# Optimization experiments

Hardware: AMD Instinct MI355X
Metric: run time of the kernel (lower is better)

## Reference

```python
import jax, jax.numpy as jnp
import numpy as np

BETA = 0.9      # membrane decay
THRESH = 1.0    # firing threshold


def _lif(x):
    """Leaky integrate-and-fire over leading time axis. x: (T, ..., C) -> spikes (T, ..., C)."""
    def step(mem, xt):
        mem = BETA * mem + xt
        s = (mem > THRESH).astype(xt.dtype)
        mem = mem - s * THRESH  # soft reset
        return mem, s
    _, spikes = jax.lax.scan(step, jnp.zeros_like(x[0]), x)
    return spikes


def setup_inputs() -> dict:
    key = jax.random.key(0)
    k1, k2, k3, k4, k5 = jax.random.split(key, 5)
    T, N, D = 4, 8192, 1024
    E, EF, TOPK = 8, 512, 2  # expert_ff = d_ff // n_experts = 4096 // 8
    x = jax.random.normal(k1, (T, N, D), dtype=jnp.float32)
    expert_indices = jax.random.randint(k2, (N, TOPK), 0, E)
    expert_weights = jax.random.uniform(k3, (N, TOPK), dtype=jnp.float32)
    up_w = jax.random.normal(k4, (E, EF, D), dtype=jnp.float32) * 0.02   # Linear(d_model, ef).weight
    down_w = jax.random.normal(k5, (E, D, EF), dtype=jnp.float32) * 0.02  # Linear(ef, d_model).weight
    return {"x": x, "expert_indices": expert_indices, "expert_weights": expert_weights,
            "up_w": up_w, "down_w": down_w}


def reference(x, expert_indices, expert_weights, up_w, down_w):
    T, N, D = x.shape
    E = up_w.shape[0]
    # Dense combine weights W[n, e] = sum_k weights[n, k] * (indices[n, k] == e)
    W = jnp.zeros((N, E), dtype=x.dtype).at[
        jnp.arange(N)[:, None], expert_indices].add(expert_weights)
    out = jnp.zeros_like(x)
    for e in range(E):  # fixed small loop over experts
        h = _lif(jnp.einsum('tnd,fd->tnf', x, up_w[e]))   # up-proj + LIF hidden
        o = _lif(jnp.einsum('tnf,df->tnd', h, down_w[e]))  # down-proj + LIF output
        out = out + o * W[:, e][None, :, None]             # weighted combine (0 for inactive)
    return out
```

## Files before the change

kernel.cpp:

```cpp
#include <hip/hip_runtime.h>
#include <stdint.h>

#define T_STEPS 4
#define NTOK    8192
#define DMODEL  1024
#define NEXP    8
#define EFF     512
#define BMT     128
#define CAPTOT  (2*NTOK + NEXP*BMT)

typedef __attribute__((ext_vector_type(8))) short bf8_t;
typedef __attribute__((ext_vector_type(4))) float f32x4;

#define MFMA(a,b,c) __builtin_amdgcn_mfma_f32_16x16x32_bf16((a),(b),(c),0,0,0)

#define SWZC(r, c) ((((c) ^ (((r) >> 1) & 3))) * 8)

typedef __attribute__((address_space(3))) unsigned int lds_uint;
typedef const __attribute__((address_space(1))) unsigned int glb_uint;
__device__ __forceinline__ void dma16(const void* g, void* l) {
    __builtin_amdgcn_global_load_lds((glb_uint*)g, (lds_uint*)l, 16, 0, 0);
}
#define S_BARRIER() __builtin_amdgcn_s_barrier()
#define SFENCE()    __builtin_amdgcn_sched_barrier(0)


__device__ __forceinline__ unsigned short bf16rn(float f) {
    unsigned u = __float_as_uint(f);
    unsigned r = u + 0x7fffu + ((u >> 16) & 1u);
    return (unsigned short)(r >> 16);
}
__device__ __forceinline__ float bf2f(unsigned short h) {
    return __uint_as_float(((unsigned)h) << 16);
}
__device__ __forceinline__ unsigned pk(unsigned short a, unsigned short b) {
    return (unsigned)a | ((unsigned)b << 16);
}

__device__ __forceinline__ void split8v(float4 va, float4 vb,
                                        unsigned short* d0, unsigned short* d1,
                                        unsigned short* d2) {
    float v[8];
    *(float4*)&v[0] = va;
    *(float4*)&v[4] = vb;
    unsigned short h[8], m[8], l[8];
#pragma unroll
    for (int i = 0; i < 8; ++i) {
        unsigned short a = bf16rn(v[i]);
        float r1 = v[i] - bf2f(a);
        unsigned short b = bf16rn(r1);
        float r2 = r1 - bf2f(b);
        h[i] = a; m[i] = b; l[i] = bf16rn(r2);
    }
    *(uint4*)d0 = make_uint4(pk(h[0],h[1]), pk(h[2],h[3]), pk(h[4],h[5]), pk(h[6],h[7]));
    *(uint4*)d1 = make_uint4(pk(m[0],m[1]), pk(m[2],m[3]), pk(m[4],m[5]), pk(m[6],m[7]));
    *(uint4*)d2 = make_uint4(pk(l[0],l[1]), pk(l[2],l[3]), pk(l[4],l[5]), pk(l[6],l[7]));
}

__device__ __forceinline__ void stage8_3limb(const float* __restrict__ src,
                                             unsigned short* d0, unsigned short* d1,
                                             unsigned short* d2) {
    float4 va = *(const float4*)(src + 0);
    float4 vb = *(const float4*)(src + 4);
    split8v(va, vb, d0, d1, d2);
}


__global__ void k_split(const float* __restrict__ w, unsigned short* __restrict__ h,
                        unsigned short* __restrict__ m, unsigned short* __restrict__ l) {
    size_t i = (size_t)(blockIdx.x * blockDim.x + threadIdx.x) * 8;
    stage8_3limb(w + i, h + i, m + i, l + i);
}


__global__ void k_count(const int* __restrict__ idx, int* __restrict__ counts) {
    int n = blockIdx.x * blockDim.x + threadIdx.x;
    if (n >= NTOK) return;
    int e0 = idx[2*n], e1 = idx[2*n+1];
    atomicAdd(&counts[e0], 1);
    if (e1 != e0) atomicAdd(&counts[e1], 1);
}

__global__ void k_prefix(const int* __restrict__ counts, int* __restrict__ offsets) {
    if (threadIdx.x == 0) {
        int o = 0;
        for (int e = 0; e < NEXP; ++e) {
            offsets[e] = o;
            o += (counts[e] + BMT - 1) / BMT * BMT;
        }
        offsets[NEXP] = o;
    }
}

__global__ void k_fill(const int* __restrict__ idx, const float* __restrict__ wts,
                       const int* __restrict__ offsets, int* __restrict__ cursors,
                       int* __restrict__ tok, float* __restrict__ wgt) {
    int n = blockIdx.x * blockDim.x + threadIdx.x;
    if (n >= NTOK) return;
    int e0 = idx[2*n], e1 = idx[2*n+1];
    float w0 = wts[2*n], w1 = wts[2*n+1];
    if (e0 == e1) w0 = __fadd_rn(w0, w1);
    int p0 = offsets[e0] + atomicAdd(&cursors[e0], 1);
    tok[p0] = n; wgt[p0] = w0;
    if (e1 != e0) {
        int p1 = offsets[e1] + atomicAdd(&cursors[e1], 1);
        tok[p1] = n; wgt[p1] = w1;
    }
}


__global__ __launch_bounds__(256, 2)
void k_up(const float* __restrict__ x,
          const unsigned short* __restrict__ uwh, const unsigned short* __restrict__ uwm,
          const unsigned short* __restrict__ uwl,
          const int* __restrict__ offsets, const int* __restrict__ tok,
          unsigned short* __restrict__ spk) {
    const int m0 = blockIdx.x * BMT;
    const int ft = blockIdx.y;
    if (m0 >= offsets[NEXP]) return;
    int e = 0;
    for (int i = 1; i < NEXP; ++i) if (m0 >= offsets[i]) e = i;

    __shared__ __align__(16) unsigned short As[3][128][32];
    __shared__ __align__(16) unsigned short Bs[2][3][128][32];

    const int tid  = threadIdx.x;
    const int lane = tid & 63, wid = tid >> 6;
    const int quad = lane >> 4, l16 = lane & 15;
    const int mw = (wid & 1) * 64, nw = (wid >> 1) * 64;

    const int r = tid >> 1, half = tid & 1;
    const int c0 = SWZC(r, half*2 + 0);
    const int c1 = SWZC(r, half*2 + 1);
    const int tokA = tok[m0 + r];
    const float* xbase = x + (size_t)tokA * DMODEL + half * 16;

    const unsigned short* wlimb[3] = { uwh, uwm, uwl };
    const size_t wrow0 = ((size_t)e * EFF + ft * 128) * DMODEL;
    const int drow  = lane >> 2;
    const int dclog = (lane & 3) ^ ((lane >> 3) & 3);

    const int kq = SWZC(l16, quad);

    f32x4 mem[4][4];
#pragma unroll
    for (int i = 0; i < 4; ++i)
#pragma unroll
        for (int j = 0; j < 4; ++j) mem[i][j] = (f32x4){0.f,0.f,0.f,0.f};

#pragma unroll
    for (int j = 0; j < 6; ++j) {
        const int limb = j >> 1, rh = j & 1;
        dma16(wlimb[limb] + wrow0 + (size_t)(rh*64 + wid*16 + drow) * DMODEL + dclog*8,
              &Bs[0][limb][rh*64 + wid*16][0]);
    }
    float4 pa[4];
#pragma unroll
    for (int i = 0; i < 4; ++i) pa[i] = ((const float4*)xbase)[i];

    int cur = 0;
    for (int t = 0; t < T_STEPS; ++t) {
        f32x4 acc[4][4];
#pragma unroll
        for (int i = 0; i < 4; ++i)
#pragma unroll
            for (int j = 0; j < 4; ++j) acc[i][j] = (f32x4){0.f,0.f,0.f,0.f};

        const float* xrow = xbase + (size_t)t * NTOK * DMODEL;

        for (int kc = 0; kc < DMODEL; kc += 32) {
            const bool last = (t == T_STEPS - 1) && (kc == DMODEL - 32);
            asm volatile("s_waitcnt lgkmcnt(0)" ::: "memory");
            SFENCE();
            S_BARRIER();
            SFENCE();
            if (!last) {
                const int nkk = (kc == DMODEL - 32) ? 0 : kc + 32;
#pragma unroll
                for (int j = 0; j < 6; ++j) {
                    const int limb = j >> 1, rh = j & 1;
                    dma16(wlimb[limb] + wrow0 + (size_t)(rh*64 + wid*16 + drow) * DMODEL
                              + nkk + dclog*8,
                          &Bs[cur ^ 1][limb][rh*64 + wid*16][0]);
                }
            }
            split8v(pa[0], pa[1], &As[0][r][c0], &As[1][r][c0], &As[2][r][c0]);
            split8v(pa[2], pa[3], &As[0][r][c1], &As[1][r][c1], &As[2][r][c1]);
            if (!last) {
                const float* nxtA = (kc == DMODEL - 32)
                    ? xbase + (size_t)(t + 1) * NTOK * DMODEL
                    : xrow + kc + 32;
#pragma unroll
                for (int i = 0; i < 4; ++i) pa[i] = ((const float4*)nxtA)[i];
                asm volatile("s_waitcnt vmcnt(10) lgkmcnt(0)" ::: "memory");
            } else {
                asm volatile("s_waitcnt vmcnt(0) lgkmcnt(0)" ::: "memory");
            }
            SFENCE();
            S_BARRIER();
            SFENCE();

            bf8_t bh[4], bm[4], bl[4];
#pragma unroll
            for (int nt = 0; nt < 4; ++nt) {
                const int nr = nw + nt*16 + l16;
                bh[nt] = *(const bf8_t*)&Bs[cur][0][nr][kq];
                bm[nt] = *(const bf8_t*)&Bs[cur][1][nr][kq];
                bl[nt] = *(const bf8_t*)&Bs[cur][2][nr][kq];
            }
#pragma unroll
            for (int mt = 0; mt < 4; ++mt) {
                const int mr = mw + mt*16 + l16;
                bf8_t ah = *(const bf8_t*)&As[0][mr][kq];
                bf8_t am = *(const bf8_t*)&As[1][mr][kq];
                bf8_t al = *(const bf8_t*)&As[2][mr][kq];
#pragma unroll
                for (int nt = 0; nt < 4; ++nt) {
                    f32x4 c = acc[mt][nt];
                    c = MFMA(ah, bh[nt], c);
                    c = MFMA(am, bh[nt], c);
                    c = MFMA(ah, bm[nt], c);
                    c = MFMA(am, bm[nt], c);
                    c = MFMA(al, bh[nt], c);
                    c = MFMA(ah, bl[nt], c);
                    acc[mt][nt] = c;
                }
            }
            cur ^= 1;
        }

#pragma unroll
        for (int mt = 0; mt < 4; ++mt)
#pragma unroll
            for (int nt = 0; nt < 4; ++nt)
#pragma unroll
                for (int reg = 0; reg < 4; ++reg) {
                    float mv = __fadd_rn(__fmul_rn(0.9f, mem[mt][nt][reg]), acc[mt][nt][reg]);
                    bool s = mv > 1.0f;
                    mem[mt][nt][reg] = __fsub_rn(mv, s ? 1.0f : 0.0f);
                    int row = m0 + mw + mt*16 + quad*4 + reg;
                    int col = ft*128 + nw + nt*16 + l16;
                    spk[((size_t)t * CAPTOT + row) * EFF + col] = s ? 0x3F80u : 0u;
                }
    }
}


__global__ __launch_bounds__(256, 2)
void k_dn(const unsigned short* __restrict__ spk,
          const unsigned short* __restrict__ dwh, const unsigned short* __restrict__ dwm,
          const unsigned short* __restrict__ dwl,
          const int* __restrict__ offsets, const int* __restrict__ tok,
          const float* __restrict__ wgt, float* __restrict__ out) {
    const int m0 = blockIdx.x * BMT;
    const int dt = blockIdx.y;
    if (m0 >= offsets[NEXP]) return;
    int e = 0;
    for (int i = 1; i < NEXP; ++i) if (m0 >= offsets[i]) e = i;

    __shared__ __align__(16) unsigned short As[2][128][32];
    __shared__ __align__(16) unsigned short Bs[2][3][128][32];

    const int tid  = threadIdx.x;
    const int lane = tid & 63, wid = tid >> 6;
    const int quad = lane >> 4, l16 = lane & 15;
    const int mw = (wid & 1) * 64, nw = (wid >> 1) * 64;

    const unsigned short* dlimb[3] = { dwh, dwm, dwl };
    const size_t drow0 = ((size_t)e * DMODEL + dt * 128) * EFF;
    const int drow  = lane >> 2;
    const int dclog = (lane & 3) ^ ((lane >> 3) & 3);

    const int kq = SWZC(l16, quad);

    f32x4 mem[4][4];
#pragma unroll
    for (int i = 0; i < 4; ++i)
#pragma unroll
        for (int j = 0; j < 4; ++j) mem[i][j] = (f32x4){0.f,0.f,0.f,0.f};

#pragma unroll
    for (int j2 = 0; j2 < 2; ++j2) {
        const int row = j2*64 + wid*16 + drow;
        dma16(spk + ((size_t)0 * CAPTOT + m0 + row) * EFF + dclog*8,
              &As[0][j2*64 + wid*16][0]);
    }
#pragma unroll
    for (int j = 0; j < 6; ++j) {
        const int limb = j >> 1, rh = j & 1;
        dma16(dlimb[limb] + drow0 + (size_t)(rh*64 + wid*16 + drow) * EFF + dclog*8,
              &Bs[0][limb][rh*64 + wid*16][0]);
    }

    int cur = 0;
    for (int t = 0; t < T_STEPS; ++t) {
        f32x4 acc[4][4];
#pragma unroll
        for (int i = 0; i < 4; ++i)
#pragma unroll
            for (int j = 0; j < 4; ++j) acc[i][j] = (f32x4){0.f,0.f,0.f,0.f};

        for (int kc = 0; kc < EFF; kc += 32) {
            const bool last = (t == T_STEPS - 1) && (kc == EFF - 32);
            asm volatile("s_waitcnt lgkmcnt(0)" ::: "memory");
            SFENCE();
            S_BARRIER();
            SFENCE();
            if (!last) {
                int ntt = t, nkk = kc + 32;
                if (nkk == EFF) { nkk = 0; ntt = t + 1; }
#pragma unroll
                for (int j2 = 0; j2 < 2; ++j2) {
                    const int row = j2*64 + wid*16 + drow;
                    dma16(spk + ((size_t)ntt * CAPTOT + m0 + row) * EFF + nkk + dclog*8,
                          &As[cur ^ 1][j2*64 + wid*16][0]);
                }
#pragma unroll
                for (int j = 0; j < 6; ++j) {
                    const int limb = j >> 1, rh = j & 1;
                    dma16(dlimb[limb] + drow0 + (size_t)(rh*64 + wid*16 + drow) * EFF
                              + nkk + dclog*8,
                          &Bs[cur ^ 1][limb][rh*64 + wid*16][0]);
                }
                asm volatile("s_waitcnt vmcnt(8)" ::: "memory");
            } else {
                asm volatile("s_waitcnt vmcnt(0)" ::: "memory");
            }
            SFENCE();
            S_BARRIER();
            SFENCE();

            bf8_t bh[4], bm[4], bl[4];
#pragma unroll
            for (int nt = 0; nt < 4; ++nt) {
                const int nr = nw + nt*16 + l16;
                bh[nt] = *(const bf8_t*)&Bs[cur][0][nr][kq];
                bm[nt] = *(const bf8_t*)&Bs[cur][1][nr][kq];
                bl[nt] = *(const bf8_t*)&Bs[cur][2][nr][kq];
            }
#pragma unroll
            for (int mt = 0; mt < 4; ++mt) {
                const int mr = mw + mt*16 + l16;
                bf8_t a = *(const bf8_t*)&As[cur][mr][kq];
#pragma unroll
                for (int nt = 0; nt < 4; ++nt) {
                    f32x4 c = acc[mt][nt];
                    c = MFMA(a, bh[nt], c);
                    c = MFMA(a, bm[nt], c);
                    c = MFMA(a, bl[nt], c);
                    acc[mt][nt] = c;
                }
            }
            cur ^= 1;
        }

#pragma unroll
        for (int mt = 0; mt < 4; ++mt) {
            const int rbase = m0 + mw + mt*16 + quad*4;
#pragma unroll
            for (int reg = 0; reg < 4; ++reg) {
                const int   n = tok[rbase + reg];
                const float w = wgt[rbase + reg];
#pragma unroll
                for (int nt = 0; nt < 4; ++nt) {
                    float mv = __fadd_rn(__fmul_rn(0.9f, mem[mt][nt][reg]), acc[mt][nt][reg]);
                    bool s = mv > 1.0f;
                    mem[mt][nt][reg] = __fsub_rn(mv, s ? 1.0f : 0.0f);
                    if (s && w != 0.0f) {
                        int col = dt*128 + nw + nt*16 + l16;
                        atomicAdd(out + ((size_t)t * NTOK + n) * DMODEL + col, w);
                    }
                }
            }
        }
    }
}


extern "C" void kernel_launch(void* const* d_in, const int* in_sizes, int n_in,
                              void* d_out, int out_size, void* d_ws, size_t ws_size,
                              hipStream_t stream) {
    const float* x      = (const float*)d_in[0];
    const int*   idx    = (const int*)  d_in[1];
    const float* wts    = (const float*)d_in[2];
    const float* up_w   = (const float*)d_in[3];
    const float* down_w = (const float*)d_in[4];
    float* out = (float*)d_out;

    char* ws = (char*)d_ws;
    int*   counts  = (int*)(ws + 0);
    int*   cursors = (int*)(ws + 32);
    int*   offsets = (int*)(ws + 64);
    int*   tok     = (int*)(ws + 128);
    float* wgt     = (float*)(ws + 128 + (size_t)CAPTOT * 4);
    unsigned short* spk = (unsigned short*)(ws + 128 + (size_t)CAPTOT * 8);

    const size_t WSPK = (size_t)T_STEPS * CAPTOT * EFF * 2;
    size_t base2 = 128 + (size_t)CAPTOT * 8 + WSPK;
    base2 = (base2 + 511) & ~(size_t)511;
    const size_t WLIMB = (size_t)NEXP * EFF * DMODEL * 2;
    unsigned short* uwh = (unsigned short*)(ws + base2);
    unsigned short* uwm = (unsigned short*)(ws + base2 + 1*WLIMB);
    unsigned short* uwl = (unsigned short*)(ws + base2 + 2*WLIMB);
    unsigned short* dwh = (unsigned short*)(ws + base2 + 3*WLIMB);
    unsigned short* dwm = (unsigned short*)(ws + base2 + 4*WLIMB);
    unsigned short* dwl = (unsigned short*)(ws + base2 + 5*WLIMB);

    hipMemsetAsync(ws, 0, 128 + (size_t)CAPTOT * 8, stream);
    hipMemsetAsync(out, 0, (size_t)out_size * sizeof(float), stream);

    const int nsplit = NEXP * EFF * DMODEL / 8 / 256;
    k_split<<<nsplit, 256, 0, stream>>>(up_w,   uwh, uwm, uwl);
    k_split<<<nsplit, 256, 0, stream>>>(down_w, dwh, dwm, dwl);

    k_count <<<(NTOK + 255) / 256, 256, 0, stream>>>(idx, counts);
    k_prefix<<<1, 64, 0, stream>>>(counts, offsets);
    k_fill  <<<(NTOK + 255) / 256, 256, 0, stream>>>(idx, wts, offsets, cursors, tok, wgt);

    dim3 gup(CAPTOT / BMT, EFF / 128);
    k_up<<<gup, 256, 0, stream>>>(x, uwh, uwm, uwl, offsets, tok, spk);

    dim3 gdn(CAPTOT / BMT, DMODEL / 128);
    k_dn<<<gdn, 256, 0, stream>>>(spk, dwh, dwm, dwl, offsets, tok, wgt, out);
}
```

Baseline: 960.1 us.

## Pre-split activations into bf16 limbs and DMA them directly into LDS

Adds a pre-pass that splits all of x into three bf16 limb arrays in the workspace, and the up-projection now loads A tiles with global-to-LDS DMA instead of per-thread float loads and in-kernel splitting. This takes the VALU split work and register staging off the GEMM's critical path. The cost is an extra full pass over x and extra workspace traffic. It also remaps block indices with a swizzle so that consecutive blocks spread across M tiles. The A DMA is issued in the same iteration it is consumed, so there is less prefetch overlap than before.

```diff
diff --git a/kernel.cpp b/kernel.cpp
--- a/kernel.cpp
+++ b/kernel.cpp
@@ -24,6 +24,8 @@
 #define S_BARRIER() __builtin_amdgcn_s_barrier()
 #define SFENCE()    __builtin_amdgcn_sched_barrier(0)
 
+__device__ __forceinline__ int swz_mb(int bx) { return (bx & 7) * 17 + (bx >> 3); }
+
 
 __device__ __forceinline__ unsigned short bf16rn(float f) {
     unsigned u = __float_as_uint(f);
@@ -37,12 +39,12 @@
     return (unsigned)a | ((unsigned)b << 16);
 }
 
-__device__ __forceinline__ void split8v(float4 va, float4 vb,
-                                        unsigned short* d0, unsigned short* d1,
-                                        unsigned short* d2) {
+__device__ __forceinline__ void stage8_3limb(const float* __restrict__ src,
+                                             unsigned short* d0, unsigned short* d1,
+                                             unsigned short* d2) {
     float v[8];
-    *(float4*)&v[0] = va;
-    *(float4*)&v[4] = vb;
+    *(float4*)&v[0] = *(const float4*)(src + 0);
+    *(float4*)&v[4] = *(const float4*)(src + 4);
     unsigned short h[8], m[8], l[8];
 #pragma unroll
     for (int i = 0; i < 8; ++i) {
@@ -55,14 +57,6 @@
     *(uint4*)d0 = make_uint4(pk(h[0],h[1]), pk(h[2],h[3]), pk(h[4],h[5]), pk(h[6],h[7]));
     *(uint4*)d1 = make_uint4(pk(m[0],m[1]), pk(m[2],m[3]), pk(m[4],m[5]), pk(m[6],m[7]));
     *(uint4*)d2 = make_uint4(pk(l[0],l[1]), pk(l[2],l[3]), pk(l[4],l[5]), pk(l[6],l[7]));
-}
-
-__device__ __forceinline__ void stage8_3limb(const float* __restrict__ src,
-                                             unsigned short* d0, unsigned short* d1,
-                                             unsigned short* d2) {
-    float4 va = *(const float4*)(src + 0);
-    float4 vb = *(const float4*)(src + 4);
-    split8v(va, vb, d0, d1, d2);
 }
 
 
@@ -110,12 +104,13 @@
 
 
 __global__ __launch_bounds__(256, 2)
-void k_up(const float* __restrict__ x,
+void k_up(const unsigned short* __restrict__ xh, const unsigned short* __restrict__ xm,
+          const unsigned short* __restrict__ xl,
           const unsigned short* __restrict__ uwh, const unsigned short* __restrict__ uwm,
           const unsigned short* __restrict__ uwl,
           const int* __restrict__ offsets, const int* __restrict__ tok,
           unsigned short* __restrict__ spk) {
-    const int m0 = blockIdx.x * BMT;
+    const int m0 = swz_mb(blockIdx.x) * BMT;
     const int ft = blockIdx.y;
     if (m0 >= offsets[NEXP]) return;
     int e = 0;
@@ -129,16 +124,13 @@
     const int quad = lane >> 4, l16 = lane & 15;
     const int mw = (wid & 1) * 64, nw = (wid >> 1) * 64;
 
-    const int r = tid >> 1, half = tid & 1;
-    const int c0 = SWZC(r, half*2 + 0);
-    const int c1 = SWZC(r, half*2 + 1);
-    const int tokA = tok[m0 + r];
-    const float* xbase = x + (size_t)tokA * DMODEL + half * 16;
-
-    const unsigned short* wlimb[3] = { uwh, uwm, uwl };
-    const size_t wrow0 = ((size_t)e * EFF + ft * 128) * DMODEL;
     const int drow  = lane >> 2;
     const int dclog = (lane & 3) ^ ((lane >> 3) & 3);
+    const unsigned short* wlimb[3] = { uwh, uwm, uwl };
+    const unsigned short* xlimb[3] = { xh, xm, xl };
+    const size_t wrow0 = ((size_t)e * EFF + ft * 128) * DMODEL;
+    const int tok0 = tok[m0 + wid*16 + drow];
+    const int tok1 = tok[m0 + 64 + wid*16 + drow];
 
     const int kq = SWZC(l16, quad);
 
@@ -154,9 +146,6 @@
         dma16(wlimb[limb] + wrow0 + (size_t)(rh*64 + wid*16 + drow) * DMODEL + dclog*8,
               &Bs[0][limb][rh*64 + wid*16][0]);
     }
-    float4 pa[4];
-#pragma unroll
-    for (int i = 0; i < 4; ++i) pa[i] = ((const float4*)xbase)[i];
 
     int cur = 0;
     for (int t = 0; t < T_STEPS; ++t) {
@@ -166,14 +155,19 @@
 #pragma unroll
             for (int j = 0; j < 4; ++j) acc[i][j] = (f32x4){0.f,0.f,0.f,0.f};
 
-        const float* xrow = xbase + (size_t)t * NTOK * DMODEL;
-
         for (int kc = 0; kc < DMODEL; kc += 32) {
             const bool last = (t == T_STEPS - 1) && (kc == DMODEL - 32);
             asm volatile("s_waitcnt lgkmcnt(0)" ::: "memory");
             SFENCE();
             S_BARRIER();
             SFENCE();
+#pragma unroll
+            for (int j = 0; j < 6; ++j) {
+                const int limb = j >> 1, rh = j & 1;
+                const int tk = rh ? tok1 : tok0;
+                dma16(xlimb[limb] + ((size_t)t * NTOK + tk) * DMODEL + kc + dclog*8,
+                      &As[limb][rh*64 + wid*16][0]);
+            }
             if (!last) {
                 const int nkk = (kc == DMODEL - 32) ? 0 : kc + 32;
 #pragma unroll
@@ -183,18 +177,9 @@
                               + nkk + dclog*8,
                           &Bs[cur ^ 1][limb][rh*64 + wid*16][0]);
                 }
-            }
-            split8v(pa[0], pa[1], &As[0][r][c0], &As[1][r][c0], &As[2][r][c0]);
-            split8v(pa[2], pa[3], &As[0][r][c1], &As[1][r][c1], &As[2][r][c1]);
-            if (!last) {
-                const float* nxtA = (kc == DMODEL - 32)
-                    ? xbase + (size_t)(t + 1) * NTOK * DMODEL
-                    : xrow + kc + 32;
-#pragma unroll
-                for (int i = 0; i < 4; ++i) pa[i] = ((const float4*)nxtA)[i];
-                asm volatile("s_waitcnt vmcnt(10) lgkmcnt(0)" ::: "memory");
+                asm volatile("s_waitcnt vmcnt(6)" ::: "memory");
             } else {
-                asm volatile("s_waitcnt vmcnt(0) lgkmcnt(0)" ::: "memory");
+                asm volatile("s_waitcnt vmcnt(0)" ::: "memory");
             }
             SFENCE();
             S_BARRIER();
@@ -252,7 +237,7 @@
           const unsigned short* __restrict__ dwl,
           const int* __restrict__ offsets, const int* __restrict__ tok,
           const float* __restrict__ wgt, float* __restrict__ out) {
-    const int m0 = blockIdx.x * BMT;
+    const int m0 = swz_mb(blockIdx.x) * BMT;
     const int dt = blockIdx.y;
     if (m0 >= offsets[NEXP]) return;
     int e = 0;
@@ -405,6 +390,11 @@
     unsigned short* dwh = (unsigned short*)(ws + base2 + 3*WLIMB);
     unsigned short* dwm = (unsigned short*)(ws + base2 + 4*WLIMB);
     unsigned short* dwl = (unsigned short*)(ws + base2 + 5*WLIMB);
+    size_t base3 = base2 + 6*WLIMB;
+    const size_t XLIMB = (size_t)T_STEPS * NTOK * DMODEL * 2;
+    unsigned short* xh = (unsigned short*)(ws + base3);
+    unsigned short* xm = (unsigned short*)(ws + base3 + 1*XLIMB);
+    unsigned short* xl = (unsigned short*)(ws + base3 + 2*XLIMB);
 
     hipMemsetAsync(ws, 0, 128 + (size_t)CAPTOT * 8, stream);
     hipMemsetAsync(out, 0, (size_t)out_size * sizeof(float), stream);
@@ -412,13 +402,15 @@
     const int nsplit = NEXP * EFF * DMODEL / 8 / 256;
     k_split<<<nsplit, 256, 0, stream>>>(up_w,   uwh, uwm, uwl);
     k_split<<<nsplit, 256, 0, stream>>>(down_w, dwh, dwm, dwl);
+    const int nsplitx = T_STEPS * NTOK * DMODEL / 8 / 256;
+    k_split<<<nsplitx, 256, 0, stream>>>(x, xh, xm, xl);
 
     k_count <<<(NTOK + 255) / 256, 256, 0, stream>>>(idx, counts);
     k_prefix<<<1, 64, 0, stream>>>(counts, offsets);
     k_fill  <<<(NTOK + 255) / 256, 256, 0, stream>>>(idx, wts, offsets, cursors, tok, wgt);
 
     dim3 gup(CAPTOT / BMT, EFF / 128);
-    k_up<<<gup, 256, 0, stream>>>(x, uwh, uwm, uwl, offsets, tok, spk);
+    k_up<<<gup, 256, 0, stream>>>(xh, xm, xl, uwh, uwm, uwl, offsets, tok, spk);
 
     dim3 gdn(CAPTOT / BMT, DMODEL / 128);
     k_dn<<<gdn, 256, 0, stream>>>(spk, dwh, dwm, dwl, offsets, tok, wgt, out);
```

New measurement: 1.235 ms. +28.7%, slower.

## Widen down-proj K tile to 64, single-buffer weights, swizzle blocks, raise MFMA priority

Applied to the files above, without the earlier changes.

In the down-projection kernel the K step grows from 32 to 64 with a new 8-way LDS swizzle. The weight limbs are now single-buffered and loaded inside the current iteration after the first barrier, instead of being prefetched one step ahead. Only the spike tile stays double-buffered. Both kernels remap block indices so neighbouring blocks are spread across experts, and raise wave priority during the MFMA section. The goal is fewer barriers per K and better scheduling, but weight-load latency is no longer hidden behind compute.

```diff
diff --git a/kernel.cpp b/kernel.cpp
--- a/kernel.cpp
+++ b/kernel.cpp
@@ -14,7 +14,8 @@
 
 #define MFMA(a,b,c) __builtin_amdgcn_mfma_f32_16x16x32_bf16((a),(b),(c),0,0,0)
 
-#define SWZC(r, c) ((((c) ^ (((r) >> 1) & 3))) * 8)
+#define SWZC(r, c)  ((((c) ^ (((r) >> 1) & 3))) * 8)
+#define SWZ64(r, c) ((((c) ^ ((r) & 7))) * 8)
 
 typedef __attribute__((address_space(3))) unsigned int lds_uint;
 typedef const __attribute__((address_space(1))) unsigned int glb_uint;
@@ -23,6 +24,8 @@
 }
 #define S_BARRIER() __builtin_amdgcn_s_barrier()
 #define SFENCE()    __builtin_amdgcn_sched_barrier(0)
+
+__device__ __forceinline__ int swz_mb(int bx) { return (bx & 7) * 17 + (bx >> 3); }
 
 
 __device__ __forceinline__ unsigned short bf16rn(float f) {
@@ -115,7 +118,7 @@
           const unsigned short* __restrict__ uwl,
           const int* __restrict__ offsets, const int* __restrict__ tok,
           unsigned short* __restrict__ spk) {
-    const int m0 = blockIdx.x * BMT;
+    const int m0 = swz_mb(blockIdx.x) * BMT;
     const int ft = blockIdx.y;
     if (m0 >= offsets[NEXP]) return;
     int e = 0;
@@ -208,6 +211,7 @@
                 bm[nt] = *(const bf8_t*)&Bs[cur][1][nr][kq];
                 bl[nt] = *(const bf8_t*)&Bs[cur][2][nr][kq];
             }
+            __builtin_amdgcn_s_setprio(1);
 #pragma unroll
             for (int mt = 0; mt < 4; ++mt) {
                 const int mr = mw + mt*16 + l16;
@@ -226,6 +230,7 @@
                     acc[mt][nt] = c;
                 }
             }
+            __builtin_amdgcn_s_setprio(0);
             cur ^= 1;
         }
 
@@ -252,14 +257,14 @@
           const unsigned short* __restrict__ dwl,
           const int* __restrict__ offsets, const int* __restrict__ tok,
           const float* __restrict__ wgt, float* __restrict__ out) {
-    const int m0 = blockIdx.x * BMT;
+    const int m0 = swz_mb(blockIdx.x) * BMT;
     const int dt = blockIdx.y;
     if (m0 >= offsets[NEXP]) return;
     int e = 0;
     for (int i = 1; i < NEXP; ++i) if (m0 >= offsets[i]) e = i;
 
-    __shared__ __align__(16) unsigned short As[2][128][32];
-    __shared__ __align__(16) unsigned short Bs[2][3][128][32];
+    __shared__ __align__(16) unsigned short As[2][128][64];
+    __shared__ __align__(16) unsigned short Bs[3][128][64];
 
     const int tid  = threadIdx.x;
     const int lane = tid & 63, wid = tid >> 6;
@@ -268,10 +273,8 @@
 
     const unsigned short* dlimb[3] = { dwh, dwm, dwl };
     const size_t drow0 = ((size_t)e * DMODEL + dt * 128) * EFF;
-    const int drow  = lane >> 2;
-    const int dclog = (lane & 3) ^ ((lane >> 3) & 3);
-
-    const int kq = SWZC(l16, quad);
+    const int drow8 = lane >> 3;
+    const int dclog = (lane & 7) ^ ((lane >> 3) & 7);
 
     f32x4 mem[4][4];
 #pragma unroll
@@ -280,16 +283,10 @@
         for (int j = 0; j < 4; ++j) mem[i][j] = (f32x4){0.f,0.f,0.f,0.f};
 
 #pragma unroll
-    for (int j2 = 0; j2 < 2; ++j2) {
-        const int row = j2*64 + wid*16 + drow;
-        dma16(spk + ((size_t)0 * CAPTOT + m0 + row) * EFF + dclog*8,
-              &As[0][j2*64 + wid*16][0]);
-    }
-#pragma unroll
-    for (int j = 0; j < 6; ++j) {
-        const int limb = j >> 1, rh = j & 1;
-        dma16(dlimb[limb] + drow0 + (size_t)(rh*64 + wid*16 + drow) * EFF + dclog*8,
-              &Bs[0][limb][rh*64 + wid*16][0]);
+    for (int j2 = 0; j2 < 4; ++j2) {
+        const int rowb = wid*32 + j2*8;
+        dma16(spk + ((size_t)(m0 + rowb + drow8)) * EFF + dclog*8,
+              &As[0][rowb][0]);
     }
 
     int cur = 0;
@@ -300,29 +297,30 @@
 #pragma unroll
             for (int j = 0; j < 4; ++j) acc[i][j] = (f32x4){0.f,0.f,0.f,0.f};
 
-        for (int kc = 0; kc < EFF; kc += 32) {
-            const bool last = (t == T_STEPS - 1) && (kc == EFF - 32);
+        for (int kc = 0; kc < EFF; kc += 64) {
+            const bool last = (t == T_STEPS - 1) && (kc == EFF - 64);
             asm volatile("s_waitcnt lgkmcnt(0)" ::: "memory");
             SFENCE();
             S_BARRIER();
             SFENCE();
+#pragma unroll
+            for (int limb = 0; limb < 3; ++limb)
+#pragma unroll
+                for (int j2 = 0; j2 < 4; ++j2) {
+                    const int rowb = wid*32 + j2*8;
+                    dma16(dlimb[limb] + drow0 + (size_t)(rowb + drow8) * EFF + kc + dclog*8,
+                          &Bs[limb][rowb][0]);
+                }
             if (!last) {
-                int ntt = t, nkk = kc + 32;
+                int ntt = t, nkk = kc + 64;
                 if (nkk == EFF) { nkk = 0; ntt = t + 1; }
 #pragma unroll
-                for (int j2 = 0; j2 < 2; ++j2) {
-                    const int row = j2*64 + wid*16 + drow;
-                    dma16(spk + ((size_t)ntt * CAPTOT + m0 + row) * EFF + nkk + dclog*8,
-                          &As[cur ^ 1][j2*64 + wid*16][0]);
-                }
-#pragma unroll
-                for (int j = 0; j < 6; ++j) {
-                    const int limb = j >> 1, rh = j & 1;
-                    dma16(dlimb[limb] + drow0 + (size_t)(rh*64 + wid*16 + drow) * EFF
-                              + nkk + dclog*8,
-                          &Bs[cur ^ 1][limb][rh*64 + wid*16][0]);
-                }
-                asm volatile("s_waitcnt vmcnt(8)" ::: "memory");
+                for (int j2 = 0; j2 < 4; ++j2) {
+                    const int rowb = wid*32 + j2*8;
+                    dma16(spk + ((size_t)ntt * CAPTOT + m0 + rowb + drow8) * EFF + nkk + dclog*8,
+                          &As[cur ^ 1][rowb][0]);
+                }
+                asm volatile("s_waitcnt vmcnt(4)" ::: "memory");
             } else {
                 asm volatile("s_waitcnt vmcnt(0)" ::: "memory");
             }
@@ -330,27 +328,33 @@
             S_BARRIER();
             SFENCE();
 
-            bf8_t bh[4], bm[4], bl[4];
-#pragma unroll
-            for (int nt = 0; nt < 4; ++nt) {
-                const int nr = nw + nt*16 + l16;
-                bh[nt] = *(const bf8_t*)&Bs[cur][0][nr][kq];
-                bm[nt] = *(const bf8_t*)&Bs[cur][1][nr][kq];
-                bl[nt] = *(const bf8_t*)&Bs[cur][2][nr][kq];
-            }
-#pragma unroll
-            for (int mt = 0; mt < 4; ++mt) {
-                const int mr = mw + mt*16 + l16;
-                bf8_t a = *(const bf8_t*)&As[cur][mr][kq];
+            __builtin_amdgcn_s_setprio(1);
+#pragma unroll
+            for (int kk = 0; kk < 2; ++kk) {
+                bf8_t bh[4], bm[4], bl[4];
 #pragma unroll
                 for (int nt = 0; nt < 4; ++nt) {
-                    f32x4 c = acc[mt][nt];
-                    c = MFMA(a, bh[nt], c);
-                    c = MFMA(a, bm[nt], c);
-                    c = MFMA(a, bl[nt], c);
-                    acc[mt][nt] = c;
-                }
-            }
+                    const int nr = nw + nt*16 + l16;
+                    const int kb = SWZ64(nr, quad + kk*4);
+                    bh[nt] = *(const bf8_t*)&Bs[0][nr][kb];
+                    bm[nt] = *(const bf8_t*)&Bs[1][nr][kb];
+                    bl[nt] = *(const bf8_t*)&Bs[2][nr][kb];
+                }
+#pragma unroll
+                for (int mt = 0; mt < 4; ++mt) {
+                    const int mr = mw + mt*16 + l16;
+                    bf8_t a = *(const bf8_t*)&As[cur][mr][SWZ64(mr, quad + kk*4)];
+#pragma unroll
+                    for (int nt = 0; nt < 4; ++nt) {
+                        f32x4 c = acc[mt][nt];
+                        c = MFMA(a, bh[nt], c);
+                        c = MFMA(a, bm[nt], c);
+                        c = MFMA(a, bl[nt], c);
+                        acc[mt][nt] = c;
+                    }
+                }
+            }
+            __builtin_amdgcn_s_setprio(0);
             cur ^= 1;
         }
 
```

Measured after the change: 1.192 ms. 24.2% more time.
